# Performance work log

Measured on AMD Instinct MI355X. Metric: run time of the kernel, lower is better.

## Reference

```python
import jax, jax.numpy as jnp
import numpy as np

B, N, D, H, L = 2, 1024, 256, 4, 6
DH = D // H          # head dim 64
RDIM = DH // 2       # AxialRotaryEmbedding dim = 32 -> output feature size DH
THETA = 0.01


def setup_inputs() -> dict:
    key = jax.random.key(0)
    ks = iter(jax.random.split(key, 80))
    def nrm(shape, s=1.0):
        return jax.random.normal(next(ks), shape, jnp.float32) * s
    size = jnp.array([1024.0, 768.0], jnp.float32)
    inp = {
        'kpts0': jax.random.uniform(next(ks), (B, N, 2), jnp.float32) * size,
        'kpts1': jax.random.uniform(next(ks), (B, N, 2), jnp.float32) * size,
        'desc0': nrm((B, N, D)),
        'desc1': nrm((B, N, D)),
        'fx': 1.0 / (THETA ** (jnp.arange(0, RDIM, 2, dtype=jnp.float32) / RDIM)),
        'fy': 1.0 / (THETA ** (jnp.arange(0, RDIM, 2, dtype=jnp.float32) / RDIM)),
    }
    s = D ** -0.5
    for p in ('s', 'c'):
        inp[f'{p}_Wqk'] = nrm((L, D, D), s); inp[f'{p}_bqk'] = jnp.zeros((L, D))
        inp[f'{p}_Wv'] = nrm((L, D, D), s);  inp[f'{p}_bv'] = jnp.zeros((L, D))
        inp[f'{p}_Wo'] = nrm((L, D, D), s);  inp[f'{p}_bo'] = jnp.zeros((L, D))
        inp[f'{p}_W1'] = nrm((L, 2 * D, 2 * D), (2 * D) ** -0.5); inp[f'{p}_b1'] = jnp.zeros((L, 2 * D))
        inp[f'{p}_g'] = jnp.ones((L, 2 * D)); inp[f'{p}_be'] = jnp.zeros((L, 2 * D))
        inp[f'{p}_W2'] = nrm((L, 2 * D, D), (2 * D) ** -0.5); inp[f'{p}_b2'] = jnp.zeros((L, D))
    inp['Wp'] = nrm((D, D), s); inp['bp'] = jnp.zeros((D,))
    inp['Wm'] = nrm((D, 1), s); inp['bm'] = jnp.zeros((1,))
    return inp


def reference(kpts0, kpts1, desc0, desc1, fx, fy,
              s_Wqk, s_bqk, s_Wv, s_bv, s_Wo, s_bo, s_W1, s_b1, s_g, s_be, s_W2, s_b2,
              c_Wqk, c_bqk, c_Wv, c_bv, c_Wo, c_bo, c_W1, c_b1, c_g, c_be, c_W2, c_b2,
              Wp, bp, Wm, bm):
    size = jnp.array([1024.0, 768.0], jnp.float32)
    norm_k = lambda k: (k - size / 2) / (size.max() / 2)
    heads = lambda t: t.reshape(t.shape[0], t.shape[1], H, DH)

    def rope(pos):  # pos [B,N,2] -> cos,sin [B,N,1,DH]
        f = jnp.concatenate([jnp.repeat(pos[..., 0:1] * fx, 2, -1),
                             jnp.repeat(pos[..., 1:2] * fy, 2, -1)], -1)[:, :, None, :]
        return jnp.cos(f), jnp.sin(f)

    def rot_half(x):  # pairs (x0,x1) -> (-x1,x0)
        return jnp.stack([-x[..., 1::2], x[..., 0::2]], -1).reshape(x.shape)

    def ln(x, g, b):
        mu = x.mean(-1, keepdims=True)
        v = ((x - mu) ** 2).mean(-1, keepdims=True)
        return (x - mu) / jnp.sqrt(v + 1e-5) * g + b

    def ffn(x, m, W1, b1, g, be, W2, b2):  # x + MLP(LN(concat(x,m)))
        h = jnp.concatenate([x, m], -1) @ W1 + b1
        return x + jax.nn.gelu(ln(h, g, be), approximate=False) @ W2 + b2

    cs0, sn0 = rope(norm_k(kpts0))
    cs1, sn1 = rope(norm_k(kpts1))
    x0, x1 = desc0, desc1
    for i in range(L):
        def self_blk(x, cs, sn):  # rotary self-attention, shared qk projection
            qk = heads(x @ s_Wqk[i] + s_bqk[i])
            qr = qk * cs + rot_half(qk) * sn
            v = heads(x @ s_Wv[i] + s_bv[i])
            a = jax.nn.softmax(jnp.einsum('bnhd,bmhd->bhnm', qr, qr) * DH ** -0.5, -1)
            m = jnp.einsum('bhnm,bmhd->bnhd', a, v).reshape(x.shape) @ s_Wo[i] + s_bo[i]
            return ffn(x, m, s_W1[i], s_b1[i], s_g[i], s_be[i], s_W2[i], s_b2[i])
        x0 = self_blk(x0, cs0, sn0)
        x1 = self_blk(x1, cs1, sn1)
        # bidirectional cross-attention (CrossTransformer math path)
        sc = (DH ** -0.5) ** 0.5
        qk0 = heads(x0 @ c_Wqk[i] + c_bqk[i]) * sc
        qk1 = heads(x1 @ c_Wqk[i] + c_bqk[i]) * sc
        v0 = heads(x0 @ c_Wv[i] + c_bv[i])
        v1 = heads(x1 @ c_Wv[i] + c_bv[i])
        sim = jnp.einsum('bnhd,bmhd->bhnm', qk0, qk1)
        m0 = jnp.einsum('bhnm,bmhd->bnhd', jax.nn.softmax(sim, -1), v1).reshape(x0.shape) @ c_Wo[i] + c_bo[i]
        m1 = jnp.einsum('bhnm,bnhd->bmhd', jax.nn.softmax(sim, 2), v0).reshape(x1.shape) @ c_Wo[i] + c_bo[i]
        x0 = ffn(x0, m0, c_W1[i], c_b1[i], c_g[i], c_be[i], c_W2[i], c_b2[i])
        x1 = ffn(x1, m1, c_W1[i], c_b1[i], c_g[i], c_be[i], c_W2[i], c_b2[i])
    # MatchAssignment: sigmoid log double softmax (temp=None, use_sqrt=False -> r=1)
    md0 = (x0 @ Wp + bp) / D ** 0.25
    md1 = (x1 @ Wp + bp) / D ** 0.25
    sim = jnp.einsum('bmd,bnd->bmn', md0, md1)
    z0 = x0 @ Wm + bm  # [B,N,1]
    z1 = x1 @ Wm + bm
    cert = jax.nn.log_sigmoid(z0) + jnp.swapaxes(jax.nn.log_sigmoid(z1), 1, 2)
    core = jax.nn.log_softmax(sim, -1) + jax.nn.log_softmax(sim, 1) + cert
    scores = jnp.zeros((sim.shape[0], N + 1, N + 1), sim.dtype)
    scores = scores.at[:, :N, :N].set(core)
    scores = scores.at[:, :N, N].set(jax.nn.log_sigmoid(-z0[..., 0]))
    scores = scores.at[:, N, :N].set(jax.nn.log_sigmoid(-z1[..., 0]))
    return scores
```

## Files before the change

### kernel.cpp

```cpp
#include <hip/hip_runtime.h>
#include <hip/hip_bf16.h>
#include <math.h>

#define NB 2
#define NN 1024
#define ND 256
#define NL 6
#define NP (NN + 1)

typedef unsigned short u16;
typedef __attribute__((ext_vector_type(8))) short bf16x8;
typedef __attribute__((ext_vector_type(4))) float f32x4;

__device__ __forceinline__ u16 f2b(float f) {
    union { float f; unsigned u; } v; v.f = f;
    unsigned r = v.u + 0x7FFFu + ((v.u >> 16) & 1u);
    return (u16)(r >> 16);
}
__device__ __forceinline__ float b2f(u16 b) {
    union { unsigned u; float f; } v; v.u = ((unsigned)b) << 16;
    return v.f;
}
__device__ __forceinline__ float logsigf(float x) {
    return (x >= 0.f) ? -log1pf(expf(-x)) : (x - log1pf(expf(x)));
}

__global__ void rope_cs_kernel(const float* __restrict__ k0p, const float* __restrict__ k1p,
                               const float* __restrict__ fx, const float* __restrict__ fy,
                               float* __restrict__ cs, float* __restrict__ sn) {
    int idx = blockIdx.x * 256 + threadIdx.x;
    int row = idx >> 6, j = idx & 63;
    const float* kp = (row < 2048) ? k0p + (size_t)row * 2 : k1p + (size_t)(row - 2048) * 2;
    float kx = kp[0], ky = kp[1];
    float f;
    if (j < 32) f = ((kx - 512.f) * (1.f / 512.f)) * fx[j >> 1];
    else        f = ((ky - 384.f) * (1.f / 512.f)) * fy[(j - 32) >> 1];
    cs[idx] = cosf(f);
    sn[idx] = sinf(f);
}

__global__ void copyconv_kernel(const float* __restrict__ d0, const float* __restrict__ d1,
                                float* __restrict__ outf, u16* __restrict__ outb) {
    int i = blockIdx.x * 256 + threadIdx.x;
    float v = (i < 524288) ? d0[i] : d1[i - 524288];
    outf[i] = v; outb[i] = f2b(v);
}

struct WP6 {
    const float* s[6];
    u16* d[6];
    unsigned long long oz[6];
};
__global__ void wconvM_kernel(WP6 w, int perT, int K, int N) {
    __shared__ float t[32][33];
    int z = blockIdx.z;
    int p = z / perT, l = z - p * perT;
    const float* W = w.s[p] + (size_t)l * K * N;
    u16* Wt = w.d[p] + (size_t)l * w.oz[p];
    int k0 = blockIdx.y * 32, n0 = blockIdx.x * 32;
    int tx = threadIdx.x, ty = threadIdx.y;
    for (int i = 0; i < 32; i += 8)
        t[ty + i][tx] = W[(size_t)(k0 + ty + i) * N + n0 + tx];
    __syncthreads();
    for (int i = 0; i < 32; i += 8)
        Wt[(size_t)(n0 + ty + i) * K + k0 + tx] = f2b(t[tx][ty + i]);
}

__global__ void biaspack_kernel(const float* __restrict__ b0, const float* __restrict__ b1,
                                float* __restrict__ out, int L) {
    int idx = blockIdx.x * 256 + threadIdx.x;
    if (idx >= L * 512) return;
    int i = idx >> 9, c = idx & 511;
    out[idx] = (c < 256) ? b0[i * 256 + c] : b1[i * 256 + c - 256];
}

__global__ __launch_bounds__(256)
void gemm_mfma(const u16* __restrict__ A, const u16* __restrict__ A2,
               const u16* __restrict__ Bt, const float* __restrict__ bias,
               const float* __restrict__ res, float* __restrict__ Cf, u16* __restrict__ Cb,
               int M, int N, int K, float scale_lo, float scale_hi,
               const float* __restrict__ csp, const float* __restrict__ snp) {
    __shared__ u16 As[2][64 * 72];
    __shared__ u16 Bs[2][64 * 72];
    int tid = threadIdx.x;
    int lane = tid & 63, wave = tid >> 6;
    int row0 = blockIdx.y * 64, col0 = blockIdx.x * 64;
    int wm = (wave >> 1) * 32, wn = (wave & 1) * 32;
    int l15 = lane & 15, l4 = lane >> 4;
    f32x4 acc[2][2] = {};
    int srl = tid >> 3, sc8 = (tid & 7) * 8;

    auto loadA = [&](int k0, int it) -> bf16x8 {
        int rr = row0 + srl + it * 32;
        int kg = k0 + sc8;
        const u16* src;
        if (A2) src = (kg < 256) ? &A[(size_t)rr * 256 + kg] : &A2[(size_t)rr * 256 + kg - 256];
        else    src = &A[(size_t)rr * K + kg];
        return *(const bf16x8*)src;
    };
    auto loadB = [&](int k0, int it) -> bf16x8 {
        return *(const bf16x8*)&Bt[(size_t)(col0 + srl + it * 32) * K + k0 + sc8];
    };

    bf16x8 rA0 = loadA(0, 0), rA1 = loadA(0, 1);
    bf16x8 rB0 = loadB(0, 0), rB1 = loadB(0, 1);
    *(bf16x8*)&As[0][srl * 72 + sc8] = rA0;
    *(bf16x8*)&As[0][(srl + 32) * 72 + sc8] = rA1;
    *(bf16x8*)&Bs[0][srl * 72 + sc8] = rB0;
    *(bf16x8*)&Bs[0][(srl + 32) * 72 + sc8] = rB1;
    __syncthreads();

    int nt = K >> 6;
    for (int t = 0; t < nt; ++t) {
        int buf = t & 1;
        bool more = (t + 1) < nt;
        if (more) {
            rA0 = loadA((t + 1) * 64, 0); rA1 = loadA((t + 1) * 64, 1);
            rB0 = loadB((t + 1) * 64, 0); rB1 = loadB((t + 1) * 64, 1);
        }
#pragma unroll
        for (int ks = 0; ks < 2; ++ks) {
            bf16x8 a0 = *(bf16x8*)&As[buf][(wm + l15) * 72 + ks * 32 + l4 * 8];
            bf16x8 a1 = *(bf16x8*)&As[buf][(wm + 16 + l15) * 72 + ks * 32 + l4 * 8];
            bf16x8 b0 = *(bf16x8*)&Bs[buf][(wn + l15) * 72 + ks * 32 + l4 * 8];
            bf16x8 b1 = *(bf16x8*)&Bs[buf][(wn + 16 + l15) * 72 + ks * 32 + l4 * 8];
            acc[0][0] = __builtin_amdgcn_mfma_f32_16x16x32_bf16(a0, b0, acc[0][0], 0, 0, 0);
            acc[0][1] = __builtin_amdgcn_mfma_f32_16x16x32_bf16(a0, b1, acc[0][1], 0, 0, 0);
            acc[1][0] = __builtin_amdgcn_mfma_f32_16x16x32_bf16(a1, b0, acc[1][0], 0, 0, 0);
            acc[1][1] = __builtin_amdgcn_mfma_f32_16x16x32_bf16(a1, b1, acc[1][1], 0, 0, 0);
        }
        if (more) {
            int nb = buf ^ 1;
            *(bf16x8*)&As[nb][srl * 72 + sc8] = rA0;
            *(bf16x8*)&As[nb][(srl + 32) * 72 + sc8] = rA1;
            *(bf16x8*)&Bs[nb][srl * 72 + sc8] = rB0;
            *(bf16x8*)&Bs[nb][(srl + 32) * 72 + sc8] = rB1;
        }
        __syncthreads();
    }
#pragma unroll
    for (int mi = 0; mi < 2; ++mi)
#pragma unroll
        for (int ni = 0; ni < 2; ++ni)
#pragma unroll
            for (int j = 0; j < 4; ++j) {
                int r = row0 + wm + mi * 16 + l4 * 4 + j;
                int c = col0 + wn + ni * 16 + l15;
                float v = acc[mi][ni][j] + (bias ? bias[c] : 0.f);
                float pn = __shfl_xor(v, 1);
                if (csp && c < 256) {
                    float cc = csp[(size_t)r * 64 + (c & 63)];
                    float ss = snp[(size_t)r * 64 + (c & 63)];
                    v = (c & 1) ? (v * cc + pn * ss) : (v * cc - pn * ss);
                }
                v *= (c < 256) ? scale_lo : scale_hi;
                if (res) v += res[(size_t)r * N + c];
                if (Cf) Cf[(size_t)r * N + c] = v;
                if (Cb) Cb[(size_t)r * N + c] = f2b(v);
            }
}

__global__ __launch_bounds__(256)
void gemm_oproj(const float* __restrict__ Op, const float* __restrict__ mp,
                const float* __restrict__ lp, const u16* __restrict__ Bt,
                const float* __restrict__ bias, u16* __restrict__ Cb) {
    __shared__ u16 As[2][64 * 72];
    __shared__ u16 Bs[2][64 * 72];
    const int N = 256, K = 256;
    int tid = threadIdx.x;
    int lane = tid & 63, wave = tid >> 6;
    int row0 = blockIdx.y * 64, col0 = blockIdx.x * 64;
    int wm = (wave >> 1) * 32, wn = (wave & 1) * 32;
    int l15 = lane & 15, l4 = lane >> 4;
    f32x4 acc[2][2] = {};
    int srl = tid >> 3, sc8 = (tid & 7) * 8;

    auto loadA = [&](int k0, int it) -> bf16x8 {
        int rg = row0 + srl + it * 32;
        int kg = k0 + sc8;
        int h = kg >> 6, d0 = kg & 63;
        int t = rg >> 11, bb = (rg >> 10) & 1, iq = rg & 1023;
        int y = t * 8 + bb * 4 + h;
        int ri = y * 1024 + iq;
        size_t base0 = (size_t)ri * 64 + d0;
        size_t base1 = base0 + (size_t)16384 * 64;
        f32x4 a0 = *(const f32x4*)&Op[base0];
        f32x4 a1 = *(const f32x4*)&Op[base0 + 4];
        f32x4 c0 = *(const f32x4*)&Op[base1];
        f32x4 c1 = *(const f32x4*)&Op[base1 + 4];
        float m0 = mp[ri], m1 = mp[16384 + ri];
        float l0 = lp[ri], l1 = lp[16384 + ri];
        float mf = fmaxf(m0, m1);
        float e0 = __expf(m0 - mf), e1 = __expf(m1 - mf);
        float inv = 1.f / (l0 * e0 + l1 * e1);
        e0 *= inv; e1 *= inv;
        u16 o[8];
#pragma unroll
        for (int e = 0; e < 4; ++e) {
            o[e] = f2b(a0[e] * e0 + c0[e] * e1);
            o[4 + e] = f2b(a1[e] * e0 + c1[e] * e1);
        }
        return *(bf16x8*)o;
    };
    auto loadB = [&](int k0, int it) -> bf16x8 {
        return *(const bf16x8*)&Bt[(size_t)(col0 + srl + it * 32) * K + k0 + sc8];
    };

    bf16x8 rA0 = loadA(0, 0), rA1 = loadA(0, 1);
    bf16x8 rB0 = loadB(0, 0), rB1 = loadB(0, 1);
    *(bf16x8*)&As[0][srl * 72 + sc8] = rA0;
    *(bf16x8*)&As[0][(srl + 32) * 72 + sc8] = rA1;
    *(bf16x8*)&Bs[0][srl * 72 + sc8] = rB0;
    *(bf16x8*)&Bs[0][(srl + 32) * 72 + sc8] = rB1;
    __syncthreads();

    for (int t = 0; t < 4; ++t) {
        int buf = t & 1;
        bool more = (t + 1) < 4;
        if (more) {
            rA0 = loadA((t + 1) * 64, 0); rA1 = loadA((t + 1) * 64, 1);
            rB0 = loadB((t + 1) * 64, 0); rB1 = loadB((t + 1) * 64, 1);
        }
#pragma unroll
        for (int ks = 0; ks < 2; ++ks) {
            bf16x8 a0 = *(bf16x8*)&As[buf][(wm + l15) * 72 + ks * 32 + l4 * 8];
            bf16x8 a1 = *(bf16x8*)&As[buf][(wm + 16 + l15) * 72 + ks * 32 + l4 * 8];
            bf16x8 b0 = *(bf16x8*)&Bs[buf][(wn + l15) * 72 + ks * 32 + l4 * 8];
            bf16x8 b1 = *(bf16x8*)&Bs[buf][(wn + 16 + l15) * 72 + ks * 32 + l4 * 8];
            acc[0][0] = __builtin_amdgcn_mfma_f32_16x16x32_bf16(a0, b0, acc[0][0], 0, 0, 0);
            acc[0][1] = __builtin_amdgcn_mfma_f32_16x16x32_bf16(a0, b1, acc[0][1], 0, 0, 0);
            acc[1][0] = __builtin_amdgcn_mfma_f32_16x16x32_bf16(a1, b0, acc[1][0], 0, 0, 0);
            acc[1][1] = __builtin_amdgcn_mfma_f32_16x16x32_bf16(a1, b1, acc[1][1], 0, 0, 0);
        }
        if (more) {
            int nb = buf ^ 1;
            *(bf16x8*)&As[nb][srl * 72 + sc8] = rA0;
            *(bf16x8*)&As[nb][(srl + 32) * 72 + sc8] = rA1;
            *(bf16x8*)&Bs[nb][srl * 72 + sc8] = rB0;
            *(bf16x8*)&Bs[nb][(srl + 32) * 72 + sc8] = rB1;
        }
        __syncthreads();
    }
#pragma unroll
    for (int mi = 0; mi < 2; ++mi)
#pragma unroll
        for (int ni = 0; ni < 2; ++ni)
#pragma unroll
            for (int j = 0; j < 4; ++j) {
                int r = row0 + wm + mi * 16 + l4 * 4 + j;
                int c = col0 + wn + ni * 16 + l15;
                Cb[(size_t)r * N + c] = f2b(acc[mi][ni][j] + bias[c]);
            }
}

__global__ __launch_bounds__(256)
void ln_gelu_wave(const u16* __restrict__ hb, const float* __restrict__ g,
                  const float* __restrict__ be, u16* __restrict__ out) {
    int wave = threadIdx.x >> 6, lane = threadIdx.x & 63;
    int row = blockIdx.x * 4 + wave;
    const u16* p = hb + (size_t)row * 512 + lane * 8;
    bf16x8 v = *(const bf16x8*)p;
    float f[8];
    float sum = 0.f, ss = 0.f;
#pragma unroll
    for (int e = 0; e < 8; ++e) {
        f[e] = b2f(((u16*)&v)[e]);
        sum += f[e]; ss += f[e] * f[e];
    }
#pragma unroll
    for (int d = 1; d < 64; d <<= 1) {
        sum += __shfl_xor(sum, d);
        ss  += __shfl_xor(ss, d);
    }
    float mu = sum * (1.f / 512.f);
    float rstd = rsqrtf(ss * (1.f / 512.f) - mu * mu + 1e-5f);
    f32x4 g0 = *(const f32x4*)&g[lane * 8];
    f32x4 g1 = *(const f32x4*)&g[lane * 8 + 4];
    f32x4 b0 = *(const f32x4*)&be[lane * 8];
    f32x4 b1 = *(const f32x4*)&be[lane * 8 + 4];
    u16 o[8];
#pragma unroll
    for (int e = 0; e < 8; ++e) {
        float gg = (e < 4) ? g0[e] : g1[e - 4];
        float bb = (e < 4) ? b0[e] : b1[e - 4];
        float y = (f[e] - mu) * rstd * gg + bb;
        o[e] = f2b(0.5f * y * (1.f + erff(y * 0.70710678118654752f)));
    }
    *(bf16x8*)(out + (size_t)row * 512 + lane * 8) = *(bf16x8*)o;
}

#define QSTR 72
#define VDSTR 1032
#define VBUFE (4 * VDSTR)

__global__ __launch_bounds__(256)
void flash_kernel(const u16* __restrict__ Qp, const u16* __restrict__ Vp,
                  float* __restrict__ Op, float* __restrict__ mp, float* __restrict__ lp,
                  int kswap) {
    __shared__ u16 Qs[64 * QSTR];
    __shared__ u16 Ks[2][64 * QSTR];
    __shared__ u16 Vs[2][VBUFE];
    __shared__ u16 Ps[64 * QSTR];
    int y = blockIdx.z;
    int half = blockIdx.y;
    int t = y >> 3, b = (y >> 2) & 1, h = y & 3;
    int qR = t * 2048 + b * 1024;
    int kt = kswap ? (1 - t) : t;
    int kR = kt * 2048 + b * 1024 + half * 512;
    int i0 = blockIdx.x * 64;
    int tid = threadIdx.x, lane = tid & 63, wave = tid >> 6;
    int l15 = lane & 15, l4 = lane >> 4;
    int wm = wave * 16;
    int srl = tid >> 3, sc8 = (tid & 7) * 8;

    const u16* Qbase = Qp + (size_t)(qR + i0) * 512 + h * 64;
    const u16* Kbase = Qp + (size_t)kR * 512 + h * 64;
    const u16* Vbase = Vp + (size_t)kR * 512 + h * 64;

#pragma unroll
    for (int it = 0; it < 2; ++it) {
        int rr = srl + it * 32;
        *(bf16x8*)&Qs[rr * QSTR + sc8] = *(const bf16x8*)&Qbase[(size_t)rr * 512 + sc8];
        *(bf16x8*)&Ks[0][rr * QSTR + sc8] = *(const bf16x8*)&Kbase[(size_t)rr * 512 + sc8];
        bf16x8 v = *(const bf16x8*)&Vbase[(size_t)rr * 512 + sc8];
        *(bf16x8*)&Vs[0][(sc8 >> 4) * VDSTR + rr * 16 + (sc8 & 15)] = v;
    }
    __syncthreads();

    bf16x8 qf[2];
    qf[0] = *(bf16x8*)&Qs[(wm + l15) * QSTR + l4 * 8];
    qf[1] = *(bf16x8*)&Qs[(wm + l15) * QSTR + 32 + l4 * 8];

    float m[4], l[4];
    f32x4 accO[4] = {};
#pragma unroll
    for (int j = 0; j < 4; ++j) { m[j] = -1e30f; l[j] = 0.f; }

    for (int j0 = 0; j0 < 512; j0 += 64) {
        int buf = (j0 >> 6) & 1;
        bool more = (j0 + 64) < 512;
        bf16x8 nK0, nK1, nV0, nV1;
        if (more) {
            nK0 = *(const bf16x8*)&Kbase[(size_t)(j0 + 64 + srl) * 512 + sc8];
            nK1 = *(const bf16x8*)&Kbase[(size_t)(j0 + 96 + srl) * 512 + sc8];
            nV0 = *(const bf16x8*)&Vbase[(size_t)(j0 + 64 + srl) * 512 + sc8];
            nV1 = *(const bf16x8*)&Vbase[(size_t)(j0 + 96 + srl) * 512 + sc8];
        }
        f32x4 accS[4] = {};
#pragma unroll
        for (int ks = 0; ks < 2; ++ks) {
#pragma unroll
            for (int n = 0; n < 4; ++n) {
                bf16x8 bb = *(bf16x8*)&Ks[buf][(n * 16 + l15) * QSTR + ks * 32 + l4 * 8];
                accS[n] = __builtin_amdgcn_mfma_f32_16x16x32_bf16(qf[ks], bb, accS[n], 0, 0, 0);
            }
        }
        float p[4][4];
#pragma unroll
        for (int j = 0; j < 4; ++j) {
            float tm = fmaxf(fmaxf(accS[0][j], accS[1][j]), fmaxf(accS[2][j], accS[3][j]));
#pragma unroll
            for (int d = 1; d < 16; d <<= 1) tm = fmaxf(tm, __shfl_xor(tm, d));
            float mnew = fmaxf(m[j], tm);
            float rr = __expf(m[j] - mnew);
            float ts = 0.f;
#pragma unroll
            for (int n = 0; n < 4; ++n) {
                float pv = __expf(accS[n][j] - mnew);
                p[n][j] = pv; ts += pv;
            }
#pragma unroll
            for (int d = 1; d < 16; d <<= 1) ts += __shfl_xor(ts, d);
            l[j] = l[j] * rr + ts;
            m[j] = mnew;
#pragma unroll
            for (int n = 0; n < 4; ++n) accO[n][j] *= rr;
        }
#pragma unroll
        for (int n = 0; n < 4; ++n) {
            int kv = n * 16 + l15;
            int c = (kv & 32) + (((kv >> 2) & 3) << 3) + (((kv >> 4) & 1) << 2) + (kv & 3);
#pragma unroll
            for (int j = 0; j < 4; ++j)
                Ps[(wm + l4 * 4 + j) * QSTR + c] = f2b(p[n][j]);
        }
#pragma unroll
        for (int ks = 0; ks < 2; ++ks) {
            bf16x8 a = *(bf16x8*)&Ps[(wm + l15) * QSTR + ks * 32 + l4 * 8];
#pragma unroll
            for (int n = 0; n < 4; ++n) {
                unsigned va = (unsigned)(size_t)(&Vs[buf][n * VDSTR]) + ks * 1024 + lane * 8;
                unsigned long long q0, q1;
                asm volatile("ds_read_b64_tr_b16 %0, %2\n\t"
                             "ds_read_b64_tr_b16 %1, %2 offset:512\n\t"
                             "s_waitcnt lgkmcnt(0)"
                             : "=&v"(q0), "=&v"(q1) : "v"(va) : "memory");
                union { unsigned long long q[2]; bf16x8 v; } uu;
                uu.q[0] = q0; uu.q[1] = q1;
                accO[n] = __builtin_amdgcn_mfma_f32_16x16x32_bf16(a, uu.v, accO[n], 0, 0, 0);
            }
        }
        if (more) {
            int nb = buf ^ 1;
            *(bf16x8*)&Ks[nb][srl * QSTR + sc8] = nK0;
            *(bf16x8*)&Ks[nb][(srl + 32) * QSTR + sc8] = nK1;
            *(bf16x8*)&Vs[nb][(sc8 >> 4) * VDSTR + srl * 16 + (sc8 & 15)] = nV0;
            *(bf16x8*)&Vs[nb][(sc8 >> 4) * VDSTR + (srl + 32) * 16 + (sc8 & 15)] = nV1;
        }
        __syncthreads();
    }
    size_t obase = (size_t)(half * 16 + y) * 1024 + i0;
#pragma unroll
    for (int n = 0; n < 4; ++n)
#pragma unroll
        for (int j = 0; j < 4; ++j) {
            int r = wm + l4 * 4 + j;
            Op[(obase + r) * 64 + n * 16 + l15] = accO[n][j];
        }
    if (l15 == 0) {
#pragma unroll
        for (int j = 0; j < 4; ++j) {
            int r = wm + l4 * 4 + j;
            mp[obase + r] = m[j];
            lp[obase + r] = l[j];
        }
    }
}

__global__ void rowstats_kernel(const float* __restrict__ S, float* __restrict__ rm,
                                float* __restrict__ rs, int ncols) {
    __shared__ float sb[256];
    int row = blockIdx.x, tid = threadIdx.x;
    const float* p = S + (size_t)row * ncols;
    float m = -1e30f;
    for (int j = tid; j < ncols; j += 256) m = fmaxf(m, p[j]);
    sb[tid] = m; __syncthreads();
    for (int s = 128; s > 0; s >>= 1) { if (tid < s) sb[tid] = fmaxf(sb[tid], sb[tid + s]); __syncthreads(); }
    m = sb[0]; __syncthreads();
    float s = 0;
    for (int j = tid; j < ncols; j += 256) s += __expf(p[j] - m);
    sb[tid] = s; __syncthreads();
    for (int st = 128; st > 0; st >>= 1) { if (tid < st) sb[tid] += sb[tid + st]; __syncthreads(); }
    if (tid == 0) { rm[row] = m; rs[row] = sb[0]; }
}

#define CSCH 8
__global__ void colstats_part(const float* __restrict__ S, float* __restrict__ pm,
                              float* __restrict__ ps) {
    int mat = blockIdx.z;
    int j = blockIdx.x * 256 + threadIdx.x;
    int r0 = blockIdx.y * (NN / CSCH);
    const float* p = S + (size_t)mat * NN * NN + (size_t)r0 * NN + j;
    float m = -1e30f;
    for (int i = 0; i < NN / CSCH; ++i) m = fmaxf(m, p[(size_t)i * NN]);
    float s = 0;
    for (int i = 0; i < NN / CSCH; ++i) s += __expf(p[(size_t)i * NN] - m);
    int o = (mat * CSCH + blockIdx.y) * NN + j;
    pm[o] = m; ps[o] = s;
}
__global__ void colstats_red(const float* __restrict__ pm, const float* __restrict__ ps,
                             float* __restrict__ cm, float* __restrict__ cs) {
    int idx = blockIdx.x * 256 + threadIdx.x;
    int mat = idx >> 10, j = idx & 1023;
    float m = -1e30f;
#pragma unroll
    for (int k = 0; k < CSCH; ++k) m = fmaxf(m, pm[(mat * CSCH + k) * NN + j]);
    float s = 0;
#pragma unroll
    for (int k = 0; k < CSCH; ++k)
        s += ps[(mat * CSCH + k) * NN + j] * __expf(pm[(mat * CSCH + k) * NN + j] - m);
    cm[idx] = m; cs[idx] = s;
}

__global__ void zproj_kernel(const float* __restrict__ X, const float* __restrict__ Wm,
                             const float* __restrict__ bm, float* __restrict__ z) {
    __shared__ float sb[256];
    int row = blockIdx.x, tid = threadIdx.x;
    float v = X[(size_t)row * 256 + tid] * Wm[tid];
    sb[tid] = v; __syncthreads();
    for (int s = 128; s > 0; s >>= 1) { if (tid < s) sb[tid] += sb[tid + s]; __syncthreads(); }
    if (tid == 0) z[row] = sb[0] + bm[0];
}

__global__ void assemble_kernel(const float* __restrict__ sim2, const float* __restrict__ z0,
                                const float* __restrict__ z1, const float* __restrict__ rm,
                                const float* __restrict__ rs, const float* __restrict__ cm,
                                const float* __restrict__ cs, float* __restrict__ out) {
    int idx = blockIdx.x * 256 + threadIdx.x;
    if (idx >= NB * NP * NP) return;
    int b = idx / (NP * NP);
    int rem = idx - b * NP * NP;
    int i = rem / NP, j = rem - i * NP;
    float v;
    if (i < NN && j < NN) {
        float s = sim2[((size_t)b * NN + i) * NN + j];
        float lr = s - rm[b * NN + i] - logf(rs[b * NN + i]);
        float lc = s - cm[b * NN + j] - logf(cs[b * NN + j]);
        v = lr + lc + logsigf(z0[b * NN + i]) + logsigf(z1[b * NN + j]);
    } else if (i < NN) {
        v = logsigf(-z0[b * NN + i]);
    } else if (j < NN) {
        v = logsigf(-z1[b * NN + j]);
    } else {
        v = 0.f;
    }
    out[idx] = v;
}

extern "C" void kernel_launch(void* const* d_in, const int* in_sizes, int n_in,
                              void* d_out, int out_size, void* d_ws, size_t ws_size,
                              hipStream_t stream) {
    auto in = [&](int i) { return (const float*)d_in[i]; };
    const float* kpts0 = in(0);
    const float* kpts1 = in(1);
    const float* desc0 = in(2);
    const float* desc1 = in(3);
    const float* fx = in(4);
    const float* fy = in(5);
    const float* sWqk = in(6);  const float* sbqk = in(7);
    const float* sWv  = in(8);  const float* sbv  = in(9);
    const float* sWo  = in(10); const float* sbo  = in(11);
    const float* sW1  = in(12); const float* sb1  = in(13);
    const float* sg   = in(14); const float* sbe  = in(15);
    const float* sW2  = in(16); const float* sb2  = in(17);
    const float* cWqk = in(18); const float* cbqk = in(19);
    const float* cWv  = in(20); const float* cbv  = in(21);
    const float* cWo  = in(22); const float* cbo  = in(23);
    const float* cW1  = in(24); const float* cb1  = in(25);
    const float* cg   = in(26); const float* cbe  = in(27);
    const float* cW2  = in(28); const float* cb2  = in(29);
    const float* Wp = in(30); const float* bp = in(31);
    const float* Wm = in(32); const float* bm = in(33);

    const int Mst = 2 * NB * NN;
    const size_t SND = (size_t)Mst * ND;

    char* base = (char*)d_ws;
    size_t off = 0;
    auto allocf = [&](size_t n) { float* p = (float*)(base + off); off += ((n * 4 + 255) & ~(size_t)255); return p; };
    auto allocb = [&](size_t n) { u16* p = (u16*)(base + off);   off += ((n * 2 + 255) & ~(size_t)255); return p; };

    float* x    = allocf(SND);
    float* cst  = allocf((size_t)Mst * 64);
    float* snt  = allocf((size_t)Mst * 64);
    float* simb = allocf((size_t)NB * NN * NN);
    float* Opb  = allocf((size_t)2 * 16384 * 64);
    float* mpb  = allocf((size_t)2 * 16384);
    float* lpb  = allocf((size_t)2 * 16384);
    float* z    = allocf(Mst);
    float* st0  = allocf(2048);
    float* st1  = allocf(2048);
    float* st2  = allocf(2048);
    float* st3  = allocf(2048);
    float* pmb  = allocf((size_t)NB * CSCH * NN);
    float* psb  = allocf((size_t)NB * CSCH * NN);
    float* bqvs = allocf((size_t)NL * 512);
    float* bqvc = allocf((size_t)NL * 512);

    u16* xb    = allocb(SND);
    u16* tQVb  = allocb((size_t)Mst * 512);
    u16* attnb = allocb(SND);
    u16* mb    = allocb(SND);
    u16* hb    = allocb((size_t)Mst * 512);
    u16* hgb   = allocb((size_t)Mst * 512);
    u16* wsqv = allocb((size_t)NL * 512 * 256);
    u16* wso  = allocb((size_t)NL * 256 * 256);
    u16* wsw1 = allocb((size_t)NL * 512 * 512);
    u16* wsw2 = allocb((size_t)NL * 512 * 256);
    u16* wcqv = allocb((size_t)NL * 512 * 256);
    u16* wco  = allocb((size_t)NL * 256 * 256);
    u16* wcw1 = allocb((size_t)NL * 512 * 512);
    u16* wcw2 = allocb((size_t)NL * 512 * 256);
    u16* wpb  = allocb((size_t)256 * 256);

    {
        WP6 wa = {};
        wa.s[0] = sWqk; wa.d[0] = wsqv;             wa.oz[0] = 512 * 256;
        wa.s[1] = sWv;  wa.d[1] = wsqv + 256 * 256; wa.oz[1] = 512 * 256;
        wa.s[2] = sWo;  wa.d[2] = wso;              wa.oz[2] = 256 * 256;
        wa.s[3] = cWqk; wa.d[3] = wcqv;             wa.oz[3] = 512 * 256;
        wa.s[4] = cWv;  wa.d[4] = wcqv + 256 * 256; wa.oz[4] = 512 * 256;
        wa.s[5] = cWo;  wa.d[5] = wco;              wa.oz[5] = 256 * 256;
        wconvM_kernel<<<dim3(8, 8, 36), dim3(32, 8), 0, stream>>>(wa, 6, 256, 256);
        WP6 wb = {};
        wb.s[0] = sW1; wb.d[0] = wsw1; wb.oz[0] = 512 * 512;
        wb.s[1] = cW1; wb.d[1] = wcw1; wb.oz[1] = 512 * 512;
        wconvM_kernel<<<dim3(16, 16, 12), dim3(32, 8), 0, stream>>>(wb, 6, 512, 512);
        WP6 wc = {};
        wc.s[0] = sW2; wc.d[0] = wsw2; wc.oz[0] = 512 * 256;
        wc.s[1] = cW2; wc.d[1] = wcw2; wc.oz[1] = 512 * 256;
        wconvM_kernel<<<dim3(8, 16, 12), dim3(32, 8), 0, stream>>>(wc, 6, 512, 256);
        WP6 wd = {};
        wd.s[0] = Wp; wd.d[0] = wpb; wd.oz[0] = 256 * 256;
        wconvM_kernel<<<dim3(8, 8, 1), dim3(32, 8), 0, stream>>>(wd, 1, 256, 256);
    }
    biaspack_kernel<<<(NL * 512 + 255) / 256, 256, 0, stream>>>(sbqk, sbv, bqvs, NL);
    biaspack_kernel<<<(NL * 512 + 255) / 256, 256, 0, stream>>>(cbqk, cbv, bqvc, NL);

    rope_cs_kernel<<<1024, 256, 0, stream>>>(kpts0, kpts1, fx, fy, cst, snt);
    copyconv_kernel<<<4096, 256, 0, stream>>>(desc0, desc1, x, xb);

    auto gemm = [&](const u16* A, const u16* A2, const u16* Bt, const float* bias,
                    const float* res, float* Cf, u16* Cb, int M, int N, int K,
                    float slo, float shi, const float* csp, const float* snp) {
        gemm_mfma<<<dim3(N / 64, M / 64), 256, 0, stream>>>(A, A2, Bt, bias, res, Cf, Cb,
                                                            M, N, K, slo, shi, csp, snp);
    };

    const float sc = 0.35355339059327379f;

    for (int i = 0; i < NL; ++i) {
        const size_t oQV = (size_t)i * 512 * 256;
        const size_t oDD = (size_t)i * 256 * 256;
        const size_t oW1 = (size_t)i * 512 * 512;
        const size_t oW2 = (size_t)i * 512 * 256;

        gemm(xb, nullptr, wsqv + oQV, bqvs + i * 512, nullptr, nullptr, tQVb,
             Mst, 512, 256, sc, 1.f, cst, snt);
        flash_kernel<<<dim3(16, 2, 16), 256, 0, stream>>>(tQVb, tQVb + 256, Opb, mpb, lpb, 0);
        gemm_oproj<<<dim3(4, 64), 256, 0, stream>>>(Opb, mpb, lpb, wso + oDD, sbo + i * ND, mb);
        gemm(xb, mb, wsw1 + oW1, sb1 + i * 512, nullptr, nullptr, hb,
             Mst, 512, 512, 1.f, 1.f, nullptr, nullptr);
        ln_gelu_wave<<<Mst / 4, 256, 0, stream>>>(hb, sg + i * 512, sbe + i * 512, hgb);
        gemm(hgb, nullptr, wsw2 + oW2, sb2 + i * ND, x, x, xb,
             Mst, 256, 512, 1.f, 1.f, nullptr, nullptr);

        gemm(xb, nullptr, wcqv + oQV, bqvc + i * 512, nullptr, nullptr, tQVb,
             Mst, 512, 256, sc, 1.f, nullptr, nullptr);
        flash_kernel<<<dim3(16, 2, 16), 256, 0, stream>>>(tQVb, tQVb + 256, Opb, mpb, lpb, 1);
        gemm_oproj<<<dim3(4, 64), 256, 0, stream>>>(Opb, mpb, lpb, wco + oDD, cbo + i * ND, mb);
        gemm(xb, mb, wcw1 + oW1, cb1 + i * 512, nullptr, nullptr, hb,
             Mst, 512, 512, 1.f, 1.f, nullptr, nullptr);
        ln_gelu_wave<<<Mst / 4, 256, 0, stream>>>(hb, cg + i * 512, cbe + i * 512, hgb);
        gemm(hgb, nullptr, wcw2 + oW2, cb2 + i * ND, x, x, xb,
             Mst, 256, 512, 1.f, 1.f, nullptr, nullptr);
    }

    gemm(xb, nullptr, wpb, bp, nullptr, nullptr, attnb,
         Mst, 256, 256, 0.25f, 0.25f, nullptr, nullptr);
    zproj_kernel<<<Mst, 256, 0, stream>>>(x, Wm, bm, z);
    for (int b = 0; b < NB; ++b) {
        gemm(attnb + (size_t)b * 1024 * 256, nullptr,
             attnb + (size_t)(2048 + b * 1024) * 256, nullptr, nullptr,
             simb + (size_t)b * NN * NN, nullptr,
             1024, 1024, 256, 1.f, 1.f, nullptr, nullptr);
    }
    rowstats_kernel<<<NB * NN, 256, 0, stream>>>(simb, st0, st1, NN);
    colstats_part<<<dim3(NN / 256, CSCH, NB), 256, 0, stream>>>(simb, pmb, psb);
    colstats_red<<<(NB * NN) / 256, 256, 0, stream>>>(pmb, psb, st2, st3);
    int total = NB * NP * NP;
    assemble_kernel<<<(total + 255) / 256, 256, 0, stream>>>(simb, z, z + 2048, st0, st1,
                                                             st2, st3, (float*)d_out);
}
```

Baseline: 1.046 ms.

## Fold output projection into FFN first layer via precomputed Wo·W1 weights

Precomputes fused weights Wo·W1[256:] and fused bias b1 + bo·W1[256:] per layer, so the attention output is fed directly into a K=512 FFN GEMM whose A operand is [x | normalized flash output]. This removes the separate o-projection GEMM launch and the intermediate message buffer in each of the 24 attention blocks. The cost is a larger fused weight-prep step and extra bf16 rounding from the pre-multiplied weights, and the softmax merge work now runs inside the wider GEMM's A loads. The bias-pack launches and Wp conversion are also consolidated into fewer kernels.

```diff
diff --git a/kernel.cpp b/kernel.cpp
--- a/kernel.cpp
+++ b/kernel.cpp
@@ -66,18 +66,93 @@
         Wt[(size_t)(n0 + ty + i) * K + k0 + tx] = f2b(t[tx][ty + i]);
 }
 
-__global__ void biaspack_kernel(const float* __restrict__ b0, const float* __restrict__ b1,
-                                float* __restrict__ out, int L) {
+__global__ void biaspack2_kernel(const float* __restrict__ sbqk, const float* __restrict__ sbv,
+                                 const float* __restrict__ cbqk, const float* __restrict__ cbv,
+                                 float* __restrict__ out) {
     int idx = blockIdx.x * 256 + threadIdx.x;
-    if (idx >= L * 512) return;
-    int i = idx >> 9, c = idx & 511;
-    out[idx] = (c < 256) ? b0[i * 256 + c] : b1[i * 256 + c - 256];
+    if (idx >= 12 * 512) return;
+    int z = idx >> 9, c = idx & 511;
+    const float* q = (z < 6) ? sbqk + z * 256 : cbqk + (z - 6) * 256;
+    const float* v = (z < 6) ? sbv + z * 256 : cbv + (z - 6) * 256;
+    out[idx] = (c < 256) ? q[c] : v[c - 256];
 }
 
 __global__ __launch_bounds__(256)
-void gemm_mfma(const u16* __restrict__ A, const u16* __restrict__ A2,
-               const u16* __restrict__ Bt, const float* __restrict__ bias,
-               const float* __restrict__ res, float* __restrict__ Cf, u16* __restrict__ Cb,
+void wfuse_kernel(const float* __restrict__ sWo, const float* __restrict__ sW1,
+                  const float* __restrict__ cWo, const float* __restrict__ cW1,
+                  u16* __restrict__ wfs, u16* __restrict__ wfc) {
+    __shared__ u16 As[64 * 72];
+    __shared__ u16 Bs[64 * 72];
+    int z = blockIdx.z;
+    const float* Wo = (z < 6) ? sWo + (size_t)z * 65536 : cWo + (size_t)(z - 6) * 65536;
+    const float* W1 = (z < 6) ? sW1 + (size_t)z * 262144 : cW1 + (size_t)(z - 6) * 262144;
+    u16* out = (z < 6) ? wfs + (size_t)z * 262144 : wfc + (size_t)(z - 6) * 262144;
+    int n0 = blockIdx.y * 64, a0 = blockIdx.x * 64;
+    int tid = threadIdx.x, lane = tid & 63, wave = tid >> 6;
+    int wm = (wave >> 1) * 32, wn = (wave & 1) * 32;
+    int l15 = lane & 15, l4 = lane >> 4;
+    f32x4 acc[2][2] = {};
+    for (int j0 = 0; j0 < 256; j0 += 64) {
+        {
+            int nl = tid & 63, jg = tid >> 6;
+#pragma unroll
+            for (int q = 0; q < 16; ++q) {
+                int j = jg * 16 + q;
+                As[nl * 72 + j] = f2b(W1[(size_t)(256 + j0 + j) * 512 + n0 + nl]);
+            }
+        }
+        {
+            int jl = tid & 63, ag = tid >> 6;
+#pragma unroll
+            for (int q = 0; q < 16; ++q) {
+                int a = ag * 16 + q;
+                Bs[a * 72 + jl] = f2b(Wo[(size_t)(a0 + a) * 256 + j0 + jl]);
+            }
+        }
+        __syncthreads();
+#pragma unroll
+        for (int ks = 0; ks < 2; ++ks) {
+            bf16x8 af0 = *(bf16x8*)&As[(wm + l15) * 72 + ks * 32 + l4 * 8];
+            bf16x8 af1 = *(bf16x8*)&As[(wm + 16 + l15) * 72 + ks * 32 + l4 * 8];
+            bf16x8 bf0 = *(bf16x8*)&Bs[(wn + l15) * 72 + ks * 32 + l4 * 8];
+            bf16x8 bf1 = *(bf16x8*)&Bs[(wn + 16 + l15) * 72 + ks * 32 + l4 * 8];
+            acc[0][0] = __builtin_amdgcn_mfma_f32_16x16x32_bf16(af0, bf0, acc[0][0], 0, 0, 0);
+            acc[0][1] = __builtin_amdgcn_mfma_f32_16x16x32_bf16(af0, bf1, acc[0][1], 0, 0, 0);
+            acc[1][0] = __builtin_amdgcn_mfma_f32_16x16x32_bf16(af1, bf0, acc[1][0], 0, 0, 0);
+            acc[1][1] = __builtin_amdgcn_mfma_f32_16x16x32_bf16(af1, bf1, acc[1][1], 0, 0, 0);
+        }
+        __syncthreads();
+    }
+#pragma unroll
+    for (int mi = 0; mi < 2; ++mi)
+#pragma unroll
+        for (int ni = 0; ni < 2; ++ni)
+#pragma unroll
+            for (int j = 0; j < 4; ++j) {
+                int r = n0 + wm + mi * 16 + l4 * 4 + j;
+                int c = a0 + wn + ni * 16 + l15;
+                out[(size_t)r * 512 + 256 + c] = f2b(acc[mi][ni][j]);
+            }
+}
+
+__global__ void bfuse_kernel(const float* __restrict__ sb1, const float* __restrict__ sbo,
+                             const float* __restrict__ sW1, const float* __restrict__ cb1,
+                             const float* __restrict__ cbo, const float* __restrict__ cW1,
+                             float* __restrict__ bfb) {
+    int z = blockIdx.y;
+    int n = blockIdx.x * 256 + threadIdx.x;
+    const float* b1 = (z < 6) ? sb1 + z * 512 : cb1 + (z - 6) * 512;
+    const float* bo = (z < 6) ? sbo + z * 256 : cbo + (z - 6) * 256;
+    const float* W1 = (z < 6) ? sW1 + (size_t)z * 262144 : cW1 + (size_t)(z - 6) * 262144;
+    float acc = b1[n];
+    for (int a = 0; a < 256; ++a) acc += bo[a] * W1[(size_t)(256 + a) * 512 + n];
+    bfb[z * 512 + n] = acc;
+}
+
+__global__ __launch_bounds__(256)
+void gemm_mfma(const u16* __restrict__ A, const u16* __restrict__ Bt,
+               const float* __restrict__ bias, const float* __restrict__ res,
+               float* __restrict__ Cf, u16* __restrict__ Cb,
                int M, int N, int K, float scale_lo, float scale_hi,
                const float* __restrict__ csp, const float* __restrict__ snp) {
     __shared__ u16 As[2][64 * 72];
@@ -91,12 +166,7 @@
     int srl = tid >> 3, sc8 = (tid & 7) * 8;
 
     auto loadA = [&](int k0, int it) -> bf16x8 {
-        int rr = row0 + srl + it * 32;
-        int kg = k0 + sc8;
-        const u16* src;
-        if (A2) src = (kg < 256) ? &A[(size_t)rr * 256 + kg] : &A2[(size_t)rr * 256 + kg - 256];
-        else    src = &A[(size_t)rr * K + kg];
-        return *(const bf16x8*)src;
+        return *(const bf16x8*)&A[(size_t)(row0 + srl + it * 32) * K + k0 + sc8];
     };
     auto loadB = [&](int k0, int it) -> bf16x8 {
         return *(const bf16x8*)&Bt[(size_t)(col0 + srl + it * 32) * K + k0 + sc8];
@@ -161,12 +231,13 @@
 }
 
 __global__ __launch_bounds__(256)
-void gemm_oproj(const float* __restrict__ Op, const float* __restrict__ mp,
-                const float* __restrict__ lp, const u16* __restrict__ Bt,
-                const float* __restrict__ bias, u16* __restrict__ Cb) {
+void gemm_w1f(const u16* __restrict__ xb, const float* __restrict__ Op,
+              const float* __restrict__ mp, const float* __restrict__ lp,
+              const u16* __restrict__ Bt, const float* __restrict__ bias,
+              u16* __restrict__ hb) {
     __shared__ u16 As[2][64 * 72];
     __shared__ u16 Bs[2][64 * 72];
-    const int N = 256, K = 256;
+    const int N = 512, K = 512;
     int tid = threadIdx.x;
     int lane = tid & 63, wave = tid >> 6;
     int row0 = blockIdx.y * 64, col0 = blockIdx.x * 64;
@@ -178,10 +249,11 @@
     auto loadA = [&](int k0, int it) -> bf16x8 {
         int rg = row0 + srl + it * 32;
         int kg = k0 + sc8;
-        int h = kg >> 6, d0 = kg & 63;
+        if (kg < 256) return *(const bf16x8*)&xb[(size_t)rg * 256 + kg];
+        int kg2 = kg - 256;
+        int h = kg2 >> 6, d0 = kg2 & 63;
         int t = rg >> 11, bb = (rg >> 10) & 1, iq = rg & 1023;
-        int y = t * 8 + bb * 4 + h;
-        int ri = y * 1024 + iq;
+        int ri = (t * 8 + bb * 4 + h) * 1024 + iq;
         size_t base0 = (size_t)ri * 64 + d0;
         size_t base1 = base0 + (size_t)16384 * 64;
         f32x4 a0 = *(const f32x4*)&Op[base0];
@@ -214,9 +286,9 @@
     *(bf16x8*)&Bs[0][(srl + 32) * 72 + sc8] = rB1;
     __syncthreads();
 
-    for (int t = 0; t < 4; ++t) {
+    for (int t = 0; t < 8; ++t) {
         int buf = t & 1;
-        bool more = (t + 1) < 4;
+        bool more = (t + 1) < 8;
         if (more) {
             rA0 = loadA((t + 1) * 64, 0); rA1 = loadA((t + 1) * 64, 1);
             rB0 = loadB((t + 1) * 64, 0); rB1 = loadB((t + 1) * 64, 1);
@@ -249,7 +321,7 @@
             for (int j = 0; j < 4; ++j) {
                 int r = row0 + wm + mi * 16 + l4 * 4 + j;
                 int c = col0 + wn + ni * 16 + l15;
-                Cb[(size_t)r * N + c] = f2b(acc[mi][ni][j] + bias[c]);
+                hb[(size_t)r * N + c] = f2b(acc[mi][ni][j] + bias[c]);
             }
 }
 
@@ -554,22 +626,19 @@
     float* st3  = allocf(2048);
     float* pmb  = allocf((size_t)NB * CSCH * NN);
     float* psb  = allocf((size_t)NB * CSCH * NN);
-    float* bqvs = allocf((size_t)NL * 512);
-    float* bqvc = allocf((size_t)NL * 512);
+    float* bqv  = allocf((size_t)12 * 512);
+    float* bfb  = allocf((size_t)12 * 512);
 
     u16* xb    = allocb(SND);
     u16* tQVb  = allocb((size_t)Mst * 512);
     u16* attnb = allocb(SND);
-    u16* mb    = allocb(SND);
     u16* hb    = allocb((size_t)Mst * 512);
     u16* hgb   = allocb((size_t)Mst * 512);
     u16* wsqv = allocb((size_t)NL * 512 * 256);
-    u16* wso  = allocb((size_t)NL * 256 * 256);
-    u16* wsw1 = allocb((size_t)NL * 512 * 512);
+    u16* wcqv = allocb((size_t)NL * 512 * 256);
+    u16* wfs  = allocb((size_t)NL * 512 * 512);
+    u16* wfc  = allocb((size_t)NL * 512 * 512);
     u16* wsw2 = allocb((size_t)NL * 512 * 256);
-    u16* wcqv = allocb((size_t)NL * 512 * 256);
-    u16* wco  = allocb((size_t)NL * 256 * 256);
-    u16* wcw1 = allocb((size_t)NL * 512 * 512);
     u16* wcw2 = allocb((size_t)NL * 512 * 256);
     u16* wpb  = allocb((size_t)256 * 256);
 
@@ -577,33 +646,30 @@
         WP6 wa = {};
         wa.s[0] = sWqk; wa.d[0] = wsqv;             wa.oz[0] = 512 * 256;
         wa.s[1] = sWv;  wa.d[1] = wsqv + 256 * 256; wa.oz[1] = 512 * 256;
-        wa.s[2] = sWo;  wa.d[2] = wso;              wa.oz[2] = 256 * 256;
-        wa.s[3] = cWqk; wa.d[3] = wcqv;             wa.oz[3] = 512 * 256;
-        wa.s[4] = cWv;  wa.d[4] = wcqv + 256 * 256; wa.oz[4] = 512 * 256;
-        wa.s[5] = cWo;  wa.d[5] = wco;              wa.oz[5] = 256 * 256;
-        wconvM_kernel<<<dim3(8, 8, 36), dim3(32, 8), 0, stream>>>(wa, 6, 256, 256);
+        wa.s[2] = cWqk; wa.d[2] = wcqv;             wa.oz[2] = 512 * 256;
+        wa.s[3] = cWv;  wa.d[3] = wcqv + 256 * 256; wa.oz[3] = 512 * 256;
+        wa.s[4] = Wp;   wa.d[4] = wpb;              wa.oz[4] = 256 * 256;
+        wconvM_kernel<<<dim3(8, 8, 25), dim3(32, 8), 0, stream>>>(wa, 6, 256, 256);
         WP6 wb = {};
-        wb.s[0] = sW1; wb.d[0] = wsw1; wb.oz[0] = 512 * 512;
-        wb.s[1] = cW1; wb.d[1] = wcw1; wb.oz[1] = 512 * 512;
-        wconvM_kernel<<<dim3(16, 16, 12), dim3(32, 8), 0, stream>>>(wb, 6, 512, 512);
+        wb.s[0] = sW1; wb.d[0] = wfs; wb.oz[0] = 512 * 512;
+        wb.s[1] = cW1; wb.d[1] = wfc; wb.oz[1] = 512 * 512;
+        wconvM_kernel<<<dim3(16, 8, 12), dim3(32, 8), 0, stream>>>(wb, 6, 512, 512);
         WP6 wc = {};
         wc.s[0] = sW2; wc.d[0] = wsw2; wc.oz[0] = 512 * 256;
         wc.s[1] = cW2; wc.d[1] = wcw2; wc.oz[1] = 512 * 256;
         wconvM_kernel<<<dim3(8, 16, 12), dim3(32, 8), 0, stream>>>(wc, 6, 512, 256);
-        WP6 wd = {};
-        wd.s[0] = Wp; wd.d[0] = wpb; wd.oz[0] = 256 * 256;
-        wconvM_kernel<<<dim3(8, 8, 1), dim3(32, 8), 0, stream>>>(wd, 1, 256, 256);
-    }
-    biaspack_kernel<<<(NL * 512 + 255) / 256, 256, 0, stream>>>(sbqk, sbv, bqvs, NL);
-    biaspack_kernel<<<(NL * 512 + 255) / 256, 256, 0, stream>>>(cbqk, cbv, bqvc, NL);
+    }
+    wfuse_kernel<<<dim3(4, 8, 12), 256, 0, stream>>>(sWo, sW1, cWo, cW1, wfs, wfc);
+    bfuse_kernel<<<dim3(2, 12), 256, 0, stream>>>(sb1, sbo, sW1, cb1, cbo, cW1, bfb);
+    biaspack2_kernel<<<(12 * 512 + 255) / 256, 256, 0, stream>>>(sbqk, sbv, cbqk, cbv, bqv);
 
     rope_cs_kernel<<<1024, 256, 0, stream>>>(kpts0, kpts1, fx, fy, cst, snt);
     copyconv_kernel<<<4096, 256, 0, stream>>>(desc0, desc1, x, xb);
 
-    auto gemm = [&](const u16* A, const u16* A2, const u16* Bt, const float* bias,
-                    const float* res, float* Cf, u16* Cb, int M, int N, int K,
+    auto gemm = [&](const u16* A, const u16* Bt, const float* bias, const float* res,
+                    float* Cf, u16* Cb, int M, int N, int K,
                     float slo, float shi, const float* csp, const float* snp) {
-        gemm_mfma<<<dim3(N / 64, M / 64), 256, 0, stream>>>(A, A2, Bt, bias, res, Cf, Cb,
+        gemm_mfma<<<dim3(N / 64, M / 64), 256, 0, stream>>>(A, Bt, bias, res, Cf, Cb,
                                                             M, N, K, slo, shi, csp, snp);
     };
 
@@ -611,36 +677,31 @@
 
     for (int i = 0; i < NL; ++i) {
         const size_t oQV = (size_t)i * 512 * 256;
-        const size_t oDD = (size_t)i * 256 * 256;
-        const size_t oW1 = (size_t)i * 512 * 512;
+        const size_t oWF = (size_t)i * 512 * 512;
         const size_t oW2 = (size_t)i * 512 * 256;
 
-        gemm(xb, nullptr, wsqv + oQV, bqvs + i * 512, nullptr, nullptr, tQVb,
+        gemm(xb, wsqv + oQV, bqv + i * 512, nullptr, nullptr, tQVb,
              Mst, 512, 256, sc, 1.f, cst, snt);
         flash_kernel<<<dim3(16, 2, 16), 256, 0, stream>>>(tQVb, tQVb + 256, Opb, mpb, lpb, 0);
-        gemm_oproj<<<dim3(4, 64), 256, 0, stream>>>(Opb, mpb, lpb, wso + oDD, sbo + i * ND, mb);
-        gemm(xb, mb, wsw1 + oW1, sb1 + i * 512, nullptr, nullptr, hb,
-             Mst, 512, 512, 1.f, 1.f, nullptr, nullptr);
+        gemm_w1f<<<dim3(8, 64), 256, 0, stream>>>(xb, Opb, mpb, lpb, wfs + oWF, bfb + i * 512, hb);
         ln_gelu_wave<<<Mst / 4, 256, 0, stream>>>(hb, sg + i * 512, sbe + i * 512, hgb);
-        gemm(hgb, nullptr, wsw2 + oW2, sb2 + i * ND, x, x, xb,
+        gemm(hgb, wsw2 + oW2, sb2 + i * ND, x, x, xb,
              Mst, 256, 512, 1.f, 1.f, nullptr, nullptr);
 
-        gemm(xb, nullptr, wcqv + oQV, bqvc + i * 512, nullptr, nullptr, tQVb,
+        gemm(xb, wcqv + oQV, bqv + (6 + i) * 512, nullptr, nullptr, tQVb,
              Mst, 512, 256, sc, 1.f, nullptr, nullptr);
         flash_kernel<<<dim3(16, 2, 16), 256, 0, stream>>>(tQVb, tQVb + 256, Opb, mpb, lpb, 1);
-        gemm_oproj<<<dim3(4, 64), 256, 0, stream>>>(Opb, mpb, lpb, wco + oDD, cbo + i * ND, mb);
-        gemm(xb, mb, wcw1 + oW1, cb1 + i * 512, nullptr, nullptr, hb,
-             Mst, 512, 512, 1.f, 1.f, nullptr, nullptr);
+        gemm_w1f<<<dim3(8, 64), 256, 0, stream>>>(xb, Opb, mpb, lpb, wfc + oWF, bfb + (6 + i) * 512, hb);
         ln_gelu_wave<<<Mst / 4, 256, 0, stream>>>(hb, cg + i * 512, cbe + i * 512, hgb);
-        gemm(hgb, nullptr, wcw2 + oW2, cb2 + i * ND, x, x, xb,
+        gemm(hgb, wcw2 + oW2, cb2 + i * ND, x, x, xb,
              Mst, 256, 512, 1.f, 1.f, nullptr, nullptr);
     }
 
-    gemm(xb, nullptr, wpb, bp, nullptr, nullptr, attnb,
+    gemm(xb, wpb, bp, nullptr, nullptr, attnb,
          Mst, 256, 256, 0.25f, 0.25f, nullptr, nullptr);
     zproj_kernel<<<Mst, 256, 0, stream>>>(x, Wm, bm, z);
     for (int b = 0; b < NB; ++b) {
-        gemm(attnb + (size_t)b * 1024 * 256, nullptr,
+        gemm(attnb + (size_t)b * 1024 * 256,
              attnb + (size_t)(2048 + b * 1024) * 256, nullptr, nullptr,
              simb + (size_t)b * NN * NN, nullptr,
              1024, 1024, 256, 1.f, 1.f, nullptr, nullptr);
```

After: 1.045 ms. About the same (-0.1%).
